# Kernel optimization log

Measured on AMD Instinct MI355X. Metric: run time of the kernel, lower is better.

## Reference

```python
import jax, jax.numpy as jnp
import numpy as np

NUM_ROUTING = 3


def squash(s, axis=-1):
    # squash(s) = |s|^2/(1+|s|^2) * s/|s|  (no epsilon, matching the torch code)
    sq = jnp.sum(s * s, axis=axis, keepdims=True)
    return sq / (1.0 + sq) * (s / jnp.sqrt(sq))


def setup_inputs() -> dict:
    key = jax.random.key(0)
    k1, k2 = jax.random.split(key)
    B, in_dim, in_num = 256, 8, 1152
    out_num, out_dim = 10, 16
    x = jax.random.normal(k1, (B, in_dim, in_num), dtype=jnp.float32)
    W = jax.random.normal(k2, (in_num, out_num, out_dim, in_dim), dtype=jnp.float32)
    return {"x": x, "W": W}


def reference(x, W):
    # x: [B, in_dim, in_num]; W: [in_num(i), out_num(j), out_dim(d), in_dim(c)]
    B = x.shape[0]
    in_num, out_num = W.shape[0], W.shape[1]
    # u_hat[i,j,b,d] = sum_c W[i,j,d,c] * x[b,c,i]
    u_hat = jnp.einsum('ijdc,bci->ijbd', W, x)
    b_ij = jnp.zeros((in_num, out_num), dtype=x.dtype)
    v = None
    for _ in range(NUM_ROUTING):
        # DGL reduce: softmax over the output-capsule axis (bucket dim)
        c = jax.nn.softmax(b_ij, axis=1)                    # [i, j]
        s = jnp.einsum('ij,ijbd->jbd', c, u_hat)            # [j, B, d]
        v = squash(s, axis=2)                               # [j, B, d]
        # edge update: b_ij += mean_b sum_d v[j,b,d] * u_hat[i,j,b,d]
        b_ij = b_ij + jnp.einsum('jbd,ijbd->ij', v, u_hat) / B
    # output: [B, out_num, out_dim, 1]
    return jnp.transpose(v, (1, 0, 2))[..., None]
```

## Files before the change

kernel.cpp:

```cpp
#include <hip/hip_runtime.h>

#define IN_NUM 1152
#define OUT_NUM 10
#define OUT_DIM 16
#define IN_DIM 8
#define NB 256
#define KTOT 9216

#define OFF_SPART 0
#define SZ_SPART (96 * OUT_NUM * OUT_DIM * NB)
#define OFF_BP (OFF_SPART + SZ_SPART)
#define SZ_BP (32 * IN_NUM * OUT_NUM)
#define OFF_VT (OFF_BP + SZ_BP)
#define SZ_VT (NB * OUT_NUM * OUT_DIM)
#define OFF_WT (OFF_VT + SZ_VT)
#define SZ_WT (OUT_NUM * OUT_DIM * KTOT)
#define OFF_WT2 (OFF_WT + SZ_WT)
#define SZ_WT2 (OUT_NUM * KTOT * OUT_DIM)

typedef short bf16x8 __attribute__((ext_vector_type(8)));
typedef float f32x4 __attribute__((ext_vector_type(4)));

__device__ __forceinline__ unsigned short f2bf(float f) {
    unsigned u = __float_as_uint(f);
    u = (u + 0x7FFFu + ((u >> 16) & 1u)) >> 16;
    return (unsigned short)u;
}

__global__ __launch_bounds__(256) void k_prep(const float* __restrict__ W,
                                              float* __restrict__ Wt,
                                              float* __restrict__ Wt2) {
    __shared__ float lds2[32][129];
    int u = blockIdx.x, t = threadIdx.x;
    int itile = u / 10, j = u - itile * 10;
    int i0 = itile * 32;
    int r0 = t >> 5, c4b = t & 31;
#pragma unroll
    for (int rr = 0; rr < 4; ++rr) {
        int rrow = rr * 8 + r0;
        float4 w4 = *reinterpret_cast<const float4*>(
            &W[(size_t)(i0 + rrow) * 1280 + j * 128 + c4b * 4]);
        lds2[rrow][c4b * 4 + 0] = w4.x; lds2[rrow][c4b * 4 + 1] = w4.y;
        lds2[rrow][c4b * 4 + 2] = w4.z; lds2[rrow][c4b * 4 + 3] = w4.w;
    }
    __syncthreads();
    int ii = t & 31, dcq = t >> 5;
#pragma unroll
    for (int rr = 0; rr < 16; ++rr) {
        int dc = rr * 8 + dcq;
        Wt[(size_t)(j * 128 + dc) * IN_NUM + i0 + ii] = lds2[ii][dc];
    }
    int d4 = t & 3, ii2 = (t >> 2) & 31, ch0 = t >> 7;
#pragma unroll
    for (int c2 = 0; c2 < 4; ++c2) {
        int c = c2 * 2 + ch0;
        float4 o;
        o.x = lds2[ii2][(d4 * 4 + 0) * 8 + c];
        o.y = lds2[ii2][(d4 * 4 + 1) * 8 + c];
        o.z = lds2[ii2][(d4 * 4 + 2) * 8 + c];
        o.w = lds2[ii2][(d4 * 4 + 3) * 8 + c];
        *reinterpret_cast<float4*>(
            &Wt2[((size_t)j * KTOT + c * IN_NUM + i0 + ii2) * OUT_DIM + d4 * 4]) = o;
    }
}

__global__ __launch_bounds__(256, 4) void k_p1(const float* __restrict__ x,
                                               const float* __restrict__ Wt2,
                                               const float* __restrict__ bp,
                                               float* __restrict__ spart, int it) {
    __shared__ float ldc[96];
    __shared__ unsigned short atT[16][100];
    int w = blockIdx.x, t = threadIdx.x;
    int g8 = w / 80, r = w - g8 * 80;
    int j = r >> 3, isp = g8 * 8 + (r & 7);
    int cch = isp / 12;
    int i0 = (isp - cch * 12) * 96;
    int k0 = isp * 96;
    if (t < 96) {
        float cv;
        if (it == 0) {
            cv = 0.1f;
        } else {
            int i = i0 + t;
            float bt_[OUT_NUM];
#pragma unroll
            for (int jp = 0; jp < OUT_NUM; ++jp) bt_[jp] = 0.f;
#pragma unroll 4
            for (int row = 0; row < 32; ++row) {
                const float2* p2 = reinterpret_cast<const float2*>(
                    &bp[(size_t)row * (IN_NUM * OUT_NUM) + i * OUT_NUM]);
#pragma unroll
                for (int q = 0; q < 5; ++q) {
                    float2 v = p2[q];
                    bt_[q * 2] += v.x; bt_[q * 2 + 1] += v.y;
                }
            }
            float m = -1e30f;
#pragma unroll
            for (int jp = 0; jp < OUT_NUM; ++jp) { bt_[jp] *= (1.f / NB); m = fmaxf(m, bt_[jp]); }
            float s = 0.f;
#pragma unroll
            for (int jp = 0; jp < OUT_NUM; ++jp) { bt_[jp] = __expf(bt_[jp] - m); s += bt_[jp]; }
            cv = bt_[j] / s;
        }
        ldc[t] = cv;
    }
    __syncthreads();
    for (int e = t; e < 1536; e += 256) {
        int d = e & 15, kk = e >> 4;
        atT[d][kk] = f2bf(ldc[kk] * Wt2[((size_t)j * KTOT + k0 + kk) * OUT_DIM + d]);
    }
    __syncthreads();
    int lane = t & 63, wv = t >> 6;
    int lg = lane >> 4, lm = lane & 15;
    bf16x8 bfr[3];
#pragma unroll
    for (int ks = 0; ks < 3; ++ks) {
        const unsigned short* p0 = &atT[lm][ks * 32 + lg * 4];
        ushort4 u0 = *reinterpret_cast<const ushort4*>(p0);
        ushort4 u1 = *reinterpret_cast<const ushort4*>(p0 + 16);
        bfr[ks][0] = (short)u0.x; bfr[ks][1] = (short)u0.y;
        bfr[ks][2] = (short)u0.z; bfr[ks][3] = (short)u0.w;
        bfr[ks][4] = (short)u1.x; bfr[ks][5] = (short)u1.y;
        bfr[ks][6] = (short)u1.z; bfr[ks][7] = (short)u1.w;
    }
    float* sp = spart + ((size_t)isp * OUT_NUM + j) * (OUT_DIM * NB);
#pragma unroll
    for (int tb = 0; tb < 4; ++tb) {
        int tbase = (wv * 4 + tb) * 16;
        const float* xr = x + (size_t)(tbase + lm) * KTOT + k0 + lg * 4;
        f32x4 acc = {0.f, 0.f, 0.f, 0.f};
#pragma unroll
        for (int ks = 0; ks < 3; ++ks) {
            float4 a0 = *reinterpret_cast<const float4*>(xr + ks * 32);
            float4 a1 = *reinterpret_cast<const float4*>(xr + ks * 32 + 16);
            bf16x8 af;
            af[0] = (short)f2bf(a0.x); af[1] = (short)f2bf(a0.y);
            af[2] = (short)f2bf(a0.z); af[3] = (short)f2bf(a0.w);
            af[4] = (short)f2bf(a1.x); af[5] = (short)f2bf(a1.y);
            af[6] = (short)f2bf(a1.z); af[7] = (short)f2bf(a1.w);
            acc = __builtin_amdgcn_mfma_f32_16x16x32_bf16(af, bfr[ks], acc, 0, 0, 0);
        }
        *reinterpret_cast<float4*>(&sp[(size_t)lm * NB + tbase + lg * 4]) =
            make_float4(acc[0], acc[1], acc[2], acc[3]);
    }
}

__global__ __launch_bounds__(256, 4) void k_p2(const float* __restrict__ spart,
                                               float* __restrict__ dst) {
    __shared__ float smem[4672];
    float (*red)[32][17] = (float (*)[32][17])smem;
    float (*nrm)[9] = (float (*)[9])(smem + 4352);
    float* cf = smem + 4640;
    int wvar = blockIdx.x, t = threadIdx.x;
    int j = wvar >> 3, bt2 = wvar & 7;
    int ie = t >> 5, bb = t & 31;
    int b = bt2 * 32 + bb;
    float acc[16];
#pragma unroll
    for (int d = 0; d < 16; ++d) acc[d] = 0.f;
    for (int q = 0; q < 12; ++q) {
        int isp = ie * 12 + q;
        const float* sp = spart + (size_t)(isp * OUT_NUM + j) * (OUT_DIM * NB) + b;
#pragma unroll
        for (int d = 0; d < 16; ++d) acc[d] += sp[d * NB];
    }
#pragma unroll
    for (int d = 0; d < 16; ++d) red[ie][bb][d] = acc[d];
    __syncthreads();
    int bb2 = t >> 3, dp = t & 7;
    float s0 = 0.f, s1 = 0.f;
#pragma unroll
    for (int e = 0; e < 8; ++e) { s0 += red[e][bb2][dp * 2]; s1 += red[e][bb2][dp * 2 + 1]; }
    nrm[bb2][dp] = s0 * s0 + s1 * s1;
    __syncthreads();
    if (t < 32) {
        float qn = 0.f;
#pragma unroll
        for (int d = 0; d < 8; ++d) qn += nrm[t][d];
        cf[t] = qn / ((1.f + qn) * sqrtf(qn));
    }
    __syncthreads();
    float cs = cf[bb2];
    float* o = dst + (size_t)(bt2 * 32 + bb2) * (OUT_NUM * OUT_DIM) + j * OUT_DIM + dp * 2;
    o[0] = s0 * cs;
    o[1] = s1 * cs;
}

__global__ __launch_bounds__(256) void k_p3(const float* __restrict__ x,
                                            const float* __restrict__ vt,
                                            const float* __restrict__ Wt,
                                            float* __restrict__ bp, int it) {
    int u = blockIdx.x, t = threadIdx.x;
    int kt = u % 36;
    int jq = u / 36;
    int j = jq >> 2, bq = jq & 3;
    int k = kt * 256 + t;
    int c = k / IN_NUM, i = k - c * IN_NUM;
    const float* xk = x + k + (size_t)(bq * 64) * KTOT;
    const float* vjb = vt + (size_t)(bq * 64) * (OUT_NUM * OUT_DIM) + j * OUT_DIM;
    float macc[16];
#pragma unroll
    for (int d = 0; d < 16; ++d) macc[d] = 0.f;
#pragma unroll 8
    for (int b = 0; b < 64; ++b) {
        float xv = xk[(size_t)b * KTOT];
        const float* vb = vjb + (size_t)b * (OUT_NUM * OUT_DIM);
#pragma unroll
        for (int d = 0; d < 16; ++d) macc[d] += vb[d] * xv;
    }
    float bs = 0.f;
#pragma unroll
    for (int d = 0; d < 16; ++d)
        bs += macc[d] * Wt[(size_t)(j * OUT_DIM + d) * KTOT + k];
    size_t idx = (size_t)(bq * 8 + c) * (IN_NUM * OUT_NUM) + (size_t)i * OUT_NUM + j;
    float prev = (it == 0) ? 0.f : bp[idx];
    bp[idx] = prev + bs;
}

extern "C" void kernel_launch(void* const* d_in, const int* in_sizes, int n_in,
                              void* d_out, int out_size, void* d_ws, size_t ws_size,
                              hipStream_t stream) {
    const float* x = (const float*)d_in[0];
    const float* W = (const float*)d_in[1];
    float* out = (float*)d_out;
    float* ws = (float*)d_ws;

    float* spart = ws + OFF_SPART;
    float* bp    = ws + OFF_BP;
    float* vt    = ws + OFF_VT;
    float* Wt    = ws + OFF_WT;
    float* Wt2   = ws + OFF_WT2;

    k_prep<<<dim3(360), dim3(256), 0, stream>>>(W, Wt, Wt2);
    for (int it = 0; it < 3; ++it) {
        k_p1<<<dim3(960), dim3(256), 0, stream>>>(x, Wt2, bp, spart, it);
        k_p2<<<dim3(80), dim3(256), 0, stream>>>(spart, it == 2 ? out : vt);
        if (it < 2) k_p3<<<dim3(1440), dim3(256), 0, stream>>>(x, vt, Wt, bp, it);
    }
}
```

Measured before the change: 121.0 us.

## Stage x tile in LDS and loop over output capsules inside k_p3

k_p3 now loads a 32-batch by 256-k tile of x into shared memory once per block and loops over all ten output capsules inside the block, instead of launching one block per capsule that re-reads x from global memory. The batch split changes from four quarters of 64 to eight groups of 32, so the partial routing-logit buffer doubles to 64 rows and k_p1's reduction sums 64 rows. This cuts repeated global x traffic but shrinks the grid from 1440 to 288 blocks, which lowers parallelism, and it adds a 32 KB LDS footprint plus a longer reduction in k_p1.

New measurement: 179.5 us. +48.3%, slower.

```diff
diff --git a/kernel.cpp b/kernel.cpp
--- a/kernel.cpp
+++ b/kernel.cpp
@@ -10,7 +10,7 @@
 #define OFF_SPART 0
 #define SZ_SPART (96 * OUT_NUM * OUT_DIM * NB)
 #define OFF_BP (OFF_SPART + SZ_SPART)
-#define SZ_BP (32 * IN_NUM * OUT_NUM)
+#define SZ_BP (64 * IN_NUM * OUT_NUM)
 #define OFF_VT (OFF_BP + SZ_BP)
 #define SZ_VT (NB * OUT_NUM * OUT_DIM)
 #define OFF_WT (OFF_VT + SZ_VT)
@@ -86,7 +86,7 @@
 #pragma unroll
             for (int jp = 0; jp < OUT_NUM; ++jp) bt_[jp] = 0.f;
 #pragma unroll 4
-            for (int row = 0; row < 32; ++row) {
+            for (int row = 0; row < 64; ++row) {
                 const float2* p2 = reinterpret_cast<const float2*>(
                     &bp[(size_t)row * (IN_NUM * OUT_NUM) + i * OUT_NUM]);
 #pragma unroll
@@ -187,35 +187,48 @@
     o[1] = s1 * cs;
 }
 
-__global__ __launch_bounds__(256) void k_p3(const float* __restrict__ x,
-                                            const float* __restrict__ vt,
-                                            const float* __restrict__ Wt,
-                                            float* __restrict__ bp, int it) {
+__global__ __launch_bounds__(256, 4) void k_p3(const float* __restrict__ x,
+                                               const float* __restrict__ vt,
+                                               const float* __restrict__ Wt,
+                                               float* __restrict__ bp, int it) {
+    __shared__ float xs[32 * 256];
     int u = blockIdx.x, t = threadIdx.x;
-    int kt = u % 36;
-    int jq = u / 36;
-    int j = jq >> 2, bq = jq & 3;
-    int k = kt * 256 + t;
+    int kt = u % 36, bq = u / 36;
+    int k0 = kt * 256;
+    int b0 = bq * 32;
+    {
+        int l = t & 63, wv = t >> 6;
+#pragma unroll
+        for (int rr = 0; rr < 8; ++rr) {
+            int row = rr * 4 + wv;
+            float4 v4 = *reinterpret_cast<const float4*>(
+                &x[(size_t)(b0 + row) * KTOT + k0 + l * 4]);
+            *reinterpret_cast<float4*>(&xs[row * 256 + l * 4]) = v4;
+        }
+    }
+    __syncthreads();
+    int k = k0 + t;
     int c = k / IN_NUM, i = k - c * IN_NUM;
-    const float* xk = x + k + (size_t)(bq * 64) * KTOT;
-    const float* vjb = vt + (size_t)(bq * 64) * (OUT_NUM * OUT_DIM) + j * OUT_DIM;
-    float macc[16];
-#pragma unroll
-    for (int d = 0; d < 16; ++d) macc[d] = 0.f;
-#pragma unroll 8
-    for (int b = 0; b < 64; ++b) {
-        float xv = xk[(size_t)b * KTOT];
-        const float* vb = vjb + (size_t)b * (OUT_NUM * OUT_DIM);
-#pragma unroll
-        for (int d = 0; d < 16; ++d) macc[d] += vb[d] * xv;
-    }
-    float bs = 0.f;
-#pragma unroll
-    for (int d = 0; d < 16; ++d)
-        bs += macc[d] * Wt[(size_t)(j * OUT_DIM + d) * KTOT + k];
-    size_t idx = (size_t)(bq * 8 + c) * (IN_NUM * OUT_NUM) + (size_t)i * OUT_NUM + j;
-    float prev = (it == 0) ? 0.f : bp[idx];
-    bp[idx] = prev + bs;
+    size_t idx = (size_t)(bq * 8 + c) * (IN_NUM * OUT_NUM) + (size_t)i * OUT_NUM;
+    for (int j = 0; j < OUT_NUM; ++j) {
+        const float* vjb = vt + (size_t)b0 * (OUT_NUM * OUT_DIM) + j * OUT_DIM;
+        float macc[16];
+#pragma unroll
+        for (int d = 0; d < 16; ++d) macc[d] = 0.f;
+#pragma unroll 4
+        for (int b = 0; b < 32; ++b) {
+            float xv = xs[b * 256 + t];
+            const float* vb = vjb + (size_t)b * (OUT_NUM * OUT_DIM);
+#pragma unroll
+            for (int d = 0; d < 16; ++d) macc[d] += vb[d] * xv;
+        }
+        float bs = 0.f;
+#pragma unroll
+        for (int d = 0; d < 16; ++d)
+            bs += macc[d] * Wt[(size_t)(j * OUT_DIM + d) * KTOT + k];
+        float prev = (it == 0) ? 0.f : bp[idx + j];
+        bp[idx + j] = prev + bs;
+    }
 }
 
 extern "C" void kernel_launch(void* const* d_in, const int* in_sizes, int n_in,
@@ -236,6 +249,6 @@
     for (int it = 0; it < 3; ++it) {
         k_p1<<<dim3(960), dim3(256), 0, stream>>>(x, Wt2, bp, spart, it);
         k_p2<<<dim3(80), dim3(256), 0, stream>>>(spart, it == 2 ? out : vt);
-        if (it < 2) k_p3<<<dim3(1440), dim3(256), 0, stream>>>(x, vt, Wt, bp, it);
-    }
-}
+        if (it < 2) k_p3<<<dim3(288), dim3(256), 0, stream>>>(x, vt, Wt, bp, it);
+    }
+}
```

## Fuse W transpose into first routing pass and tile agreement kernel via LDS

Applied to the files above, without the earlier changes.

Removes the separate k_prep launch: in iteration 0, k_p1 reads raw W directly, writes the transposed Wt and Wt2 copies needed later, and builds its bf16 operand from the raw values. k_p3 is restructured to stage 32 batches of x and v into shared memory and compute all 5 output capsules per thread half, so it reuses x across j instead of re-reading global memory per (j, batch-quarter). The b partial buffer grows from 32 to 64 slices, so k_p1 now sums twice as many rows. The fused prep writes use scattered, uncoalesced stores, and k_p3 uses more LDS per block.

Result: slower. 162.6 us (+34.3%).

```diff
diff --git a/kernel.cpp b/kernel.cpp
--- a/kernel.cpp
+++ b/kernel.cpp
@@ -10,7 +10,7 @@
 #define OFF_SPART 0
 #define SZ_SPART (96 * OUT_NUM * OUT_DIM * NB)
 #define OFF_BP (OFF_SPART + SZ_SPART)
-#define SZ_BP (32 * IN_NUM * OUT_NUM)
+#define SZ_BP (64 * IN_NUM * OUT_NUM)
 #define OFF_VT (OFF_BP + SZ_BP)
 #define SZ_VT (NB * OUT_NUM * OUT_DIM)
 #define OFF_WT (OFF_VT + SZ_VT)
@@ -27,45 +27,10 @@
     return (unsigned short)u;
 }
 
-__global__ __launch_bounds__(256) void k_prep(const float* __restrict__ W,
-                                              float* __restrict__ Wt,
-                                              float* __restrict__ Wt2) {
-    __shared__ float lds2[32][129];
-    int u = blockIdx.x, t = threadIdx.x;
-    int itile = u / 10, j = u - itile * 10;
-    int i0 = itile * 32;
-    int r0 = t >> 5, c4b = t & 31;
-#pragma unroll
-    for (int rr = 0; rr < 4; ++rr) {
-        int rrow = rr * 8 + r0;
-        float4 w4 = *reinterpret_cast<const float4*>(
-            &W[(size_t)(i0 + rrow) * 1280 + j * 128 + c4b * 4]);
-        lds2[rrow][c4b * 4 + 0] = w4.x; lds2[rrow][c4b * 4 + 1] = w4.y;
-        lds2[rrow][c4b * 4 + 2] = w4.z; lds2[rrow][c4b * 4 + 3] = w4.w;
-    }
-    __syncthreads();
-    int ii = t & 31, dcq = t >> 5;
-#pragma unroll
-    for (int rr = 0; rr < 16; ++rr) {
-        int dc = rr * 8 + dcq;
-        Wt[(size_t)(j * 128 + dc) * IN_NUM + i0 + ii] = lds2[ii][dc];
-    }
-    int d4 = t & 3, ii2 = (t >> 2) & 31, ch0 = t >> 7;
-#pragma unroll
-    for (int c2 = 0; c2 < 4; ++c2) {
-        int c = c2 * 2 + ch0;
-        float4 o;
-        o.x = lds2[ii2][(d4 * 4 + 0) * 8 + c];
-        o.y = lds2[ii2][(d4 * 4 + 1) * 8 + c];
-        o.z = lds2[ii2][(d4 * 4 + 2) * 8 + c];
-        o.w = lds2[ii2][(d4 * 4 + 3) * 8 + c];
-        *reinterpret_cast<float4*>(
-            &Wt2[((size_t)j * KTOT + c * IN_NUM + i0 + ii2) * OUT_DIM + d4 * 4]) = o;
-    }
-}
-
 __global__ __launch_bounds__(256, 4) void k_p1(const float* __restrict__ x,
-                                               const float* __restrict__ Wt2,
+                                               const float* __restrict__ W,
+                                               float* __restrict__ Wt,
+                                               float* __restrict__ Wt2,
                                                const float* __restrict__ bp,
                                                float* __restrict__ spart, int it) {
     __shared__ float ldc[96];
@@ -76,39 +41,43 @@
     int cch = isp / 12;
     int i0 = (isp - cch * 12) * 96;
     int k0 = isp * 96;
-    if (t < 96) {
-        float cv;
-        if (it == 0) {
-            cv = 0.1f;
-        } else {
-            int i = i0 + t;
-            float bt_[OUT_NUM];
-#pragma unroll
-            for (int jp = 0; jp < OUT_NUM; ++jp) bt_[jp] = 0.f;
+    if (it > 0 && t < 96) {
+        int i = i0 + t;
+        float bt_[OUT_NUM];
+#pragma unroll
+        for (int jp = 0; jp < OUT_NUM; ++jp) bt_[jp] = 0.f;
 #pragma unroll 4
-            for (int row = 0; row < 32; ++row) {
-                const float2* p2 = reinterpret_cast<const float2*>(
-                    &bp[(size_t)row * (IN_NUM * OUT_NUM) + i * OUT_NUM]);
-#pragma unroll
-                for (int q = 0; q < 5; ++q) {
-                    float2 v = p2[q];
-                    bt_[q * 2] += v.x; bt_[q * 2 + 1] += v.y;
-                }
+        for (int row = 0; row < 64; ++row) {
+            const float2* p2 = reinterpret_cast<const float2*>(
+                &bp[(size_t)row * (IN_NUM * OUT_NUM) + i * OUT_NUM]);
+#pragma unroll
+            for (int q = 0; q < 5; ++q) {
+                float2 v = p2[q];
+                bt_[q * 2] += v.x; bt_[q * 2 + 1] += v.y;
             }
-            float m = -1e30f;
-#pragma unroll
-            for (int jp = 0; jp < OUT_NUM; ++jp) { bt_[jp] *= (1.f / NB); m = fmaxf(m, bt_[jp]); }
-            float s = 0.f;
-#pragma unroll
-            for (int jp = 0; jp < OUT_NUM; ++jp) { bt_[jp] = __expf(bt_[jp] - m); s += bt_[jp]; }
-            cv = bt_[j] / s;
-        }
-        ldc[t] = cv;
-    }
-    __syncthreads();
-    for (int e = t; e < 1536; e += 256) {
-        int d = e & 15, kk = e >> 4;
-        atT[d][kk] = f2bf(ldc[kk] * Wt2[((size_t)j * KTOT + k0 + kk) * OUT_DIM + d]);
+        }
+        float m = -1e30f;
+#pragma unroll
+        for (int jp = 0; jp < OUT_NUM; ++jp) { bt_[jp] *= (1.f / NB); m = fmaxf(m, bt_[jp]); }
+        float s = 0.f;
+#pragma unroll
+        for (int jp = 0; jp < OUT_NUM; ++jp) { bt_[jp] = __expf(bt_[jp] - m); s += bt_[jp]; }
+        ldc[t] = bt_[j] / s;
+    }
+    __syncthreads();
+    if (it == 0) {
+        for (int e = t; e < 1536; e += 256) {
+            int d = e / 96, kk = e - d * 96;
+            float raw = W[(size_t)(i0 + kk) * 1280 + j * 128 + d * 8 + cch];
+            Wt[(size_t)(j * 128 + d * 8 + cch) * IN_NUM + i0 + kk] = raw;
+            Wt2[((size_t)j * KTOT + cch * IN_NUM + i0 + kk) * OUT_DIM + d] = raw;
+            atT[d][kk] = f2bf(0.1f * raw);
+        }
+    } else {
+        for (int e = t; e < 1536; e += 256) {
+            int d = e & 15, kk = e >> 4;
+            atT[d][kk] = f2bf(ldc[kk] * Wt2[((size_t)j * KTOT + k0 + kk) * OUT_DIM + d]);
+        }
     }
     __syncthreads();
     int lane = t & 63, wv = t >> 6;
@@ -187,35 +156,52 @@
     o[1] = s1 * cs;
 }
 
-__global__ __launch_bounds__(256) void k_p3(const float* __restrict__ x,
-                                            const float* __restrict__ vt,
-                                            const float* __restrict__ Wt,
-                                            float* __restrict__ bp, int it) {
+__global__ __launch_bounds__(256, 4) void k_p3(const float* __restrict__ x,
+                                               const float* __restrict__ vt,
+                                               const float* __restrict__ Wt,
+                                               float* __restrict__ bp, int it) {
+    __shared__ float xs[32 * 128];
+    __shared__ float vs[32 * 160];
     int u = blockIdx.x, t = threadIdx.x;
-    int kt = u % 36;
-    int jq = u / 36;
-    int j = jq >> 2, bq = jq & 3;
-    int k = kt * 256 + t;
+    int kt = u % 72, bs = u / 72;
+    int k0 = kt * 128, b0 = bs * 32;
+#pragma unroll
+    for (int p = 0; p < 4; ++p) {
+        int e = p * 256 + t;
+        int row = e >> 5, c4 = e & 31;
+        *reinterpret_cast<float4*>(&xs[row * 128 + c4 * 4]) =
+            *reinterpret_cast<const float4*>(&x[(size_t)(b0 + row) * KTOT + k0 + c4 * 4]);
+    }
+    {
+        const float4* src = reinterpret_cast<const float4*>(vt + (size_t)b0 * 160);
+        float4* dst4 = reinterpret_cast<float4*>(vs);
+#pragma unroll
+        for (int p = 0; p < 5; ++p) dst4[p * 256 + t] = src[p * 256 + t];
+    }
+    __syncthreads();
+    int jh = t >> 7, kl = t & 127;
+    int k = k0 + kl;
     int c = k / IN_NUM, i = k - c * IN_NUM;
-    const float* xk = x + k + (size_t)(bq * 64) * KTOT;
-    const float* vjb = vt + (size_t)(bq * 64) * (OUT_NUM * OUT_DIM) + j * OUT_DIM;
-    float macc[16];
-#pragma unroll
-    for (int d = 0; d < 16; ++d) macc[d] = 0.f;
+    size_t idx = ((size_t)(bs * 8 + c) * IN_NUM + i) * OUT_NUM + jh * 5;
+#pragma unroll
+    for (int jj = 0; jj < 5; ++jj) {
+        int j = jh * 5 + jj;
+        float macc[16];
+#pragma unroll
+        for (int d = 0; d < 16; ++d) macc[d] = 0.f;
 #pragma unroll 8
-    for (int b = 0; b < 64; ++b) {
-        float xv = xk[(size_t)b * KTOT];
-        const float* vb = vjb + (size_t)b * (OUT_NUM * OUT_DIM);
-#pragma unroll
-        for (int d = 0; d < 16; ++d) macc[d] += vb[d] * xv;
-    }
-    float bs = 0.f;
-#pragma unroll
-    for (int d = 0; d < 16; ++d)
-        bs += macc[d] * Wt[(size_t)(j * OUT_DIM + d) * KTOT + k];
-    size_t idx = (size_t)(bq * 8 + c) * (IN_NUM * OUT_NUM) + (size_t)i * OUT_NUM + j;
-    float prev = (it == 0) ? 0.f : bp[idx];
-    bp[idx] = prev + bs;
+        for (int b = 0; b < 32; ++b) {
+            float xv = xs[b * 128 + kl];
+            const float* vb = &vs[b * 160 + j * 16];
+#pragma unroll
+            for (int d = 0; d < 16; ++d) macc[d] += vb[d] * xv;
+        }
+        float bsum = 0.f;
+#pragma unroll
+        for (int d = 0; d < 16; ++d)
+            bsum += macc[d] * Wt[(size_t)(j * OUT_DIM + d) * KTOT + k];
+        bp[idx + jj] = (it == 0) ? bsum : (bp[idx + jj] + bsum);
+    }
 }
 
 extern "C" void kernel_launch(void* const* d_in, const int* in_sizes, int n_in,
@@ -232,10 +218,9 @@
     float* Wt    = ws + OFF_WT;
     float* Wt2   = ws + OFF_WT2;
 
-    k_prep<<<dim3(360), dim3(256), 0, stream>>>(W, Wt, Wt2);
     for (int it = 0; it < 3; ++it) {
-        k_p1<<<dim3(960), dim3(256), 0, stream>>>(x, Wt2, bp, spart, it);
+        k_p1<<<dim3(960), dim3(256), 0, stream>>>(x, W, Wt, Wt2, bp, spart, it);
         k_p2<<<dim3(80), dim3(256), 0, stream>>>(spart, it == 2 ? out : vt);
-        if (it < 2) k_p3<<<dim3(1440), dim3(256), 0, stream>>>(x, vt, Wt, bp, it);
-    }
-}
+        if (it < 2) k_p3<<<dim3(576), dim3(256), 0, stream>>>(x, vt, Wt, bp, it);
+    }
+}
```
